# Optimization experiments

Measured on AMD Instinct MI355X. Metric: run time of the kernel, lower is better.

The kernel has to match this reference:

```python
import jax, jax.numpy as jnp
import numpy as np

NEG_SLOPE = 0.2  # PyG GATConv default negative_slope
EPS = 1e-16


def gat_conv(x, src, dst, num_nodes, W, att_src, att_dst, bias, concat):
    """PyG-style GATConv (eval mode, no dropout). att_*: [H, C]."""
    H, C = att_src.shape
    h = (x @ W).reshape(num_nodes, H, C)                      # [N,H,C]
    a_s = jnp.einsum('nhc,hc->nh', h, att_src)                # [N,H]
    a_d = jnp.einsum('nhc,hc->nh', h, att_dst)                # [N,H]
    e = jax.nn.leaky_relu(a_s[src] + a_d[dst], NEG_SLOPE)     # [E,H]
    # segment softmax over edges grouped by destination node
    m = jax.lax.stop_gradient(jax.ops.segment_max(e, dst, num_segments=num_nodes))
    ex = jnp.exp(e - m[dst])
    denom = jax.ops.segment_sum(ex, dst, num_segments=num_nodes)
    alpha = ex / (denom[dst] + EPS)                           # [E,H]
    msg = h[src] * alpha[:, :, None]                          # [E,H,C]
    out = jax.ops.segment_sum(msg, dst, num_segments=num_nodes)  # [N,H,C]
    out = out.reshape(num_nodes, H * C) if concat else out.mean(axis=1)
    return out + bias


def setup_inputs() -> dict:
    key = jax.random.key(0)
    ks = jax.random.split(key, 12)
    N, E = 65536, 1310720
    IN, HID, OUT, HEADS = 768, 128, 2, 8
    C1 = HID // HEADS  # 16
    s = 0.05
    return {
        'x': jax.random.normal(ks[0], (N, IN), jnp.float32),
        'edge_index': jax.random.randint(ks[1], (2, E), 0, N, jnp.int64),
        'W1': jax.random.normal(ks[2], (IN, HEADS * C1), jnp.float32) * s,
        'att_src1': jax.random.normal(ks[3], (HEADS, C1), jnp.float32) * s,
        'att_dst1': jax.random.normal(ks[4], (HEADS, C1), jnp.float32) * s,
        'b1': jnp.zeros((HID,), jnp.float32),
        'Wp': jax.random.normal(ks[5], (IN, HID), jnp.float32) * s,
        'bp': jnp.zeros((HID,), jnp.float32),
        'W2': jax.random.normal(ks[6], (HID, OUT), jnp.float32) * s,
        'att_src2': jax.random.normal(ks[7], (1, OUT), jnp.float32) * s,
        'att_dst2': jax.random.normal(ks[8], (1, OUT), jnp.float32) * s,
        'b2': jnp.zeros((OUT,), jnp.float32),
    }


def reference(x, edge_index, W1, att_src1, att_dst1, b1, Wp, bp, W2, att_src2, att_dst2, b2):
    N = x.shape[0]
    loops = jnp.arange(N, dtype=edge_index.dtype)  # add_self_loops=True
    src = jnp.concatenate([edge_index[0], loops])
    dst = jnp.concatenate([edge_index[1], loops])
    # eval mode: dropout is identity
    h1 = gat_conv(x, src, dst, N, W1, att_src1, att_dst1, b1, concat=True)
    h = jax.nn.elu(h1 + x @ Wp + bp)  # residual projection + ELU
    return gat_conv(h, src, dst, N, W2, att_src2, att_dst2, b2, concat=False)
```

## Files before the change

### kernel.cpp

```cpp
#include <hip/hip_runtime.h>
#include <hip/hip_bf16.h>
#include <math.h>

#define NEG_SLOPE 0.2f

typedef __attribute__((ext_vector_type(8))) short short8;
typedef __attribute__((ext_vector_type(4))) float float4v;

__device__ __forceinline__ unsigned f2bf(float f) {
  unsigned u = __builtin_bit_cast(unsigned, f);
  return (u + 0x7fffu + ((u >> 16) & 1u)) >> 16;
}
__device__ __forceinline__ float bflo(unsigned u) {
  return __builtin_bit_cast(float, u << 16);
}
__device__ __forceinline__ float bfhi(unsigned u) {
  return __builtin_bit_cast(float, u & 0xffff0000u);
}

__global__ __launch_bounds__(256) void convert_w(const float* __restrict__ W1,
                                                 const float* __restrict__ Wp,
                                                 short* __restrict__ Wt) {
  int k = blockIdx.x;
  int c = threadIdx.x;
  float v = (c < 128) ? W1[k * 128 + c] : Wp[k * 128 + (c - 128)];
  Wt[(size_t)c * 768 + k] = (short)f2bf(v);
}

__global__ __launch_bounds__(256) void gemm_mfma(const float* __restrict__ x,
                                                 const short* __restrict__ Wt,
                                                 float* __restrict__ proj,
                                                 unsigned* __restrict__ h1bf) {
  __shared__ short As[64][40];
  __shared__ short Bs[256][40];
  const int tid = threadIdx.x;
  const int wave = tid >> 6, lane = tid & 63;
  const int l15 = lane & 15, l4 = lane >> 4;
  const int row0 = blockIdx.x * 64;

  const int ar = tid >> 3;
  const int ak = (tid & 7) * 4;
  const int bc = tid >> 2;
  const int bk = (tid & 3) * 8;

  float4v acc[4][4] = {};

  for (int k0 = 0; k0 < 768; k0 += 32) {
#pragma unroll
    for (int i = 0; i < 2; i++) {
      int r = i * 32 + ar;
      float4 f = *(const float4*)&x[(size_t)(row0 + r) * 768 + k0 + ak];
      uint2 p;
      p.x = f2bf(f.x) | (f2bf(f.y) << 16);
      p.y = f2bf(f.z) | (f2bf(f.w) << 16);
      *(uint2*)&As[r][ak] = p;
    }
#pragma unroll
    for (int i = 0; i < 4; i++) {
      int c = i * 64 + bc;
      uint4 v = *(const uint4*)&Wt[(size_t)c * 768 + k0 + bk];
      *(uint4*)&Bs[c][bk] = v;
    }
    __syncthreads();

    short8 afr[4];
#pragma unroll
    for (int rt = 0; rt < 4; rt++)
      afr[rt] = *(const short8*)&As[rt * 16 + l15][l4 * 8];
#pragma unroll
    for (int ct = 0; ct < 4; ct++) {
      short8 bfr = *(const short8*)&Bs[wave * 64 + ct * 16 + l15][l4 * 8];
#pragma unroll
      for (int rt = 0; rt < 4; rt++)
        acc[rt][ct] =
            __builtin_amdgcn_mfma_f32_16x16x32_bf16(afr[rt], bfr, acc[rt][ct], 0, 0, 0);
    }
    __syncthreads();
  }

  const int colbase = wave * 64;
  if (wave < 2) {
#pragma unroll
    for (int ct = 0; ct < 4; ct++) {
      const int c = colbase + ct * 16 + l15;
#pragma unroll
      for (int rt = 0; rt < 4; rt++) {
#pragma unroll
        for (int r = 0; r < 4; r++) {
          const int R = row0 + rt * 16 + l4 * 4 + r;
          unsigned u = f2bf(acc[rt][ct][r]);
          unsigned up = __shfl_xor(u, 1);
          if ((l15 & 1) == 0) h1bf[(size_t)R * 64 + (c >> 1)] = u | (up << 16);
        }
      }
    }
  } else {
#pragma unroll
    for (int ct = 0; ct < 4; ct++) {
      const int c = colbase - 128 + ct * 16 + l15;
#pragma unroll
      for (int rt = 0; rt < 4; rt++) {
#pragma unroll
        for (int r = 0; r < 4; r++) {
          const int R = row0 + rt * 16 + l4 * 4 + r;
          proj[(size_t)R * 128 + c] = acc[rt][ct][r];
        }
      }
    }
  }
}

__global__ __launch_bounds__(256) void attn1b(const uint4* __restrict__ h1bf4,
                                              const float* __restrict__ att_src1,
                                              const float* __restrict__ att_dst1,
                                              float* __restrict__ a_s1,
                                              float* __restrict__ a_d1) {
  const int t = blockIdx.x * 256 + threadIdx.x;
  const int n = t >> 3, h = t & 7;
  uint4 q0 = h1bf4[(size_t)n * 16 + h * 2];
  uint4 q1 = h1bf4[(size_t)n * 16 + h * 2 + 1];
  float v[16];
  v[0] = bflo(q0.x); v[1] = bfhi(q0.x); v[2] = bflo(q0.y); v[3] = bfhi(q0.y);
  v[4] = bflo(q0.z); v[5] = bfhi(q0.z); v[6] = bflo(q0.w); v[7] = bfhi(q0.w);
  v[8] = bflo(q1.x); v[9] = bfhi(q1.x); v[10] = bflo(q1.y); v[11] = bfhi(q1.y);
  v[12] = bflo(q1.z); v[13] = bfhi(q1.z); v[14] = bflo(q1.w); v[15] = bfhi(q1.w);
  float as = 0.f, ad = 0.f;
#pragma unroll
  for (int i = 0; i < 16; i++) {
    as += v[i] * att_src1[h * 16 + i];
    ad += v[i] * att_dst1[h * 16 + i];
  }
  a_s1[t] = as;
  a_d1[t] = ad;
}

__global__ void init_counts(int* counts, int N) {
  int i = blockIdx.x * blockDim.x + threadIdx.x;
  if (i < N) counts[i] = 1;
}

__global__ void hist_kernel(const int* __restrict__ dst, int* counts, int E) {
  int i = blockIdx.x * blockDim.x + threadIdx.x;
  int base = i * 4;
  if (base + 3 < E) {
    int4 d = *(const int4*)&dst[base];
    atomicAdd(&counts[d.x], 1);
    atomicAdd(&counts[d.y], 1);
    atomicAdd(&counts[d.z], 1);
    atomicAdd(&counts[d.w], 1);
  } else {
    for (int j = base; j < E; j++) atomicAdd(&counts[dst[j]], 1);
  }
}

__global__ __launch_bounds__(256) void scan_a(const int* __restrict__ counts,
                                              int* offsets, int* bsum) {
  __shared__ int s[256];
  int t = threadIdx.x, idx = blockIdx.x * 256 + t;
  int v = counts[idx];
  s[t] = v;
  __syncthreads();
  for (int d = 1; d < 256; d <<= 1) {
    int x = (t >= d) ? s[t - d] : 0;
    __syncthreads();
    s[t] += x;
    __syncthreads();
  }
  offsets[idx] = s[t] - v;
  if (t == 255) bsum[blockIdx.x] = s[t];
}

__global__ __launch_bounds__(256) void scan_b(int* bsum) {
  __shared__ int s[256];
  int t = threadIdx.x;
  int v = bsum[t];
  s[t] = v;
  __syncthreads();
  for (int d = 1; d < 256; d <<= 1) {
    int x = (t >= d) ? s[t - d] : 0;
    __syncthreads();
    s[t] += x;
    __syncthreads();
  }
  bsum[t] = s[t] - v;
}

__global__ __launch_bounds__(256) void scan_c(int* offsets, const int* bsum,
                                              int* cursor, int* sortedsrc,
                                              int N, int Etot) {
  int t = threadIdx.x, idx = blockIdx.x * 256 + t;
  int off = offsets[idx] + bsum[blockIdx.x];
  offsets[idx] = off;
  sortedsrc[off] = idx;
  cursor[idx] = off + 1;
  if (idx == 0) offsets[N] = Etot;
}

__global__ void scatter_edges(const int* __restrict__ src,
                              const int* __restrict__ dst, int* cursor,
                              int* sortedsrc, int E) {
  int i = blockIdx.x * blockDim.x + threadIdx.x;
  int base = i * 4;
  if (base + 3 < E) {
    int4 s = *(const int4*)&src[base];
    int4 d = *(const int4*)&dst[base];
    sortedsrc[atomicAdd(&cursor[d.x], 1)] = s.x;
    sortedsrc[atomicAdd(&cursor[d.y], 1)] = s.y;
    sortedsrc[atomicAdd(&cursor[d.z], 1)] = s.z;
    sortedsrc[atomicAdd(&cursor[d.w], 1)] = s.w;
  } else {
    for (int j = base; j < E; j++)
      sortedsrc[atomicAdd(&cursor[dst[j]], 1)] = src[j];
  }
}

__global__ __launch_bounds__(256) void agg1_fused(
    const uint4* __restrict__ h1bf4, const float* __restrict__ proj,
    const float* __restrict__ a_s1, const float* __restrict__ a_d1,
    const int* __restrict__ offsets, const int* __restrict__ sortedsrc,
    const float* __restrict__ b1, const float* __restrict__ bp,
    const float* __restrict__ W2, const float* __restrict__ att_s2,
    const float* __restrict__ att_d2, float* __restrict__ h2,
    float* __restrict__ as2, float* __restrict__ ad2) {
  const int t = threadIdx.x;
  const int n = blockIdx.x * 16 + (t >> 4);
  const int k = t & 15;
  const int hd = k >> 1;
  const float ad = a_d1[n * 8 + hd];
  const int begin = offsets[n], end = offsets[n + 1];
  float acc[8] = {};
  float aw = 0.f;
  int j = begin;
  for (; j + 4 <= end; j += 4) {
    int s0 = sortedsrc[j], s1 = sortedsrc[j + 1];
    int s2 = sortedsrc[j + 2], s3 = sortedsrc[j + 3];
    float e0 = a_s1[s0 * 8 + hd], e1 = a_s1[s1 * 8 + hd];
    float e2 = a_s1[s2 * 8 + hd], e3 = a_s1[s3 * 8 + hd];
    uint4 q0 = h1bf4[(size_t)s0 * 16 + k];
    uint4 q1 = h1bf4[(size_t)s1 * 16 + k];
    uint4 q2 = h1bf4[(size_t)s2 * 16 + k];
    uint4 q3 = h1bf4[(size_t)s3 * 16 + k];
    e0 += ad; e1 += ad; e2 += ad; e3 += ad;
    float w0 = __expf(e0 > 0.f ? e0 : NEG_SLOPE * e0);
    float w1 = __expf(e1 > 0.f ? e1 : NEG_SLOPE * e1);
    float w2 = __expf(e2 > 0.f ? e2 : NEG_SLOPE * e2);
    float w3 = __expf(e3 > 0.f ? e3 : NEG_SLOPE * e3);
    acc[0] += w0 * bflo(q0.x) + w1 * bflo(q1.x) + w2 * bflo(q2.x) + w3 * bflo(q3.x);
    acc[1] += w0 * bfhi(q0.x) + w1 * bfhi(q1.x) + w2 * bfhi(q2.x) + w3 * bfhi(q3.x);
    acc[2] += w0 * bflo(q0.y) + w1 * bflo(q1.y) + w2 * bflo(q2.y) + w3 * bflo(q3.y);
    acc[3] += w0 * bfhi(q0.y) + w1 * bfhi(q1.y) + w2 * bfhi(q2.y) + w3 * bfhi(q3.y);
    acc[4] += w0 * bflo(q0.z) + w1 * bflo(q1.z) + w2 * bflo(q2.z) + w3 * bflo(q3.z);
    acc[5] += w0 * bfhi(q0.z) + w1 * bfhi(q1.z) + w2 * bfhi(q2.z) + w3 * bfhi(q3.z);
    acc[6] += w0 * bflo(q0.w) + w1 * bflo(q1.w) + w2 * bflo(q2.w) + w3 * bflo(q3.w);
    acc[7] += w0 * bfhi(q0.w) + w1 * bfhi(q1.w) + w2 * bfhi(q2.w) + w3 * bfhi(q3.w);
    aw += (w0 + w1) + (w2 + w3);
  }
  for (; j < end; j++) {
    int s0 = sortedsrc[j];
    float e0 = a_s1[s0 * 8 + hd] + ad;
    uint4 q0 = h1bf4[(size_t)s0 * 16 + k];
    float w0 = __expf(e0 > 0.f ? e0 : NEG_SLOPE * e0);
    acc[0] += w0 * bflo(q0.x);
    acc[1] += w0 * bfhi(q0.x);
    acc[2] += w0 * bflo(q0.y);
    acc[3] += w0 * bfhi(q0.y);
    acc[4] += w0 * bflo(q0.z);
    acc[5] += w0 * bfhi(q0.z);
    acc[6] += w0 * bflo(q0.w);
    acc[7] += w0 * bfhi(q0.w);
    aw += w0;
  }
  const float inv = 1.f / (aw + 1e-16f);
  const float4 pj0 = *(const float4*)&proj[(size_t)n * 128 + k * 8];
  const float4 pj1 = *(const float4*)&proj[(size_t)n * 128 + k * 8 + 4];
  const float4 b1a = *(const float4*)&b1[k * 8];
  const float4 b1b = *(const float4*)&b1[k * 8 + 4];
  const float4 bpa = *(const float4*)&bp[k * 8];
  const float4 bpb = *(const float4*)&bp[k * 8 + 4];
  float v[8];
  v[0] = acc[0] * inv + pj0.x + b1a.x + bpa.x;
  v[1] = acc[1] * inv + pj0.y + b1a.y + bpa.y;
  v[2] = acc[2] * inv + pj0.z + b1a.z + bpa.z;
  v[3] = acc[3] * inv + pj0.w + b1a.w + bpa.w;
  v[4] = acc[4] * inv + pj1.x + b1b.x + bpb.x;
  v[5] = acc[5] * inv + pj1.y + b1b.y + bpb.y;
  v[6] = acc[6] * inv + pj1.z + b1b.z + bpb.z;
  v[7] = acc[7] * inv + pj1.w + b1b.w + bpb.w;
  float p0 = 0.f, p1 = 0.f;
#pragma unroll
  for (int i = 0; i < 8; i++) {
    float vi = v[i] > 0.f ? v[i] : (__expf(v[i]) - 1.f);
    float2 w2 = *(const float2*)&W2[(k * 8 + i) * 2];
    p0 += vi * w2.x;
    p1 += vi * w2.y;
  }
#pragma unroll
  for (int off = 8; off; off >>= 1) {
    p0 += __shfl_xor(p0, off);
    p1 += __shfl_xor(p1, off);
  }
  if (k == 0) {
    h2[2 * n] = p0;
    h2[2 * n + 1] = p1;
    as2[n] = p0 * att_s2[0] + p1 * att_s2[1];
    ad2[n] = p0 * att_d2[0] + p1 * att_d2[1];
  }
}

__global__ __launch_bounds__(256) void agg2(
    const float* __restrict__ h2, const float* __restrict__ as2,
    const float* __restrict__ ad2, const int* __restrict__ offsets,
    const int* __restrict__ sortedsrc, const float* __restrict__ b2,
    float* __restrict__ out, int N) {
  const int node = blockIdx.x * 16 + (threadIdx.x >> 4);
  const int lane = threadIdx.x & 15;
  const int begin = offsets[node], end = offsets[node + 1];
  const float ad = ad2[node];
  float acc0 = 0.f, acc1 = 0.f, aw = 0.f;
  for (int j = begin + lane; j < end; j += 16) {
    int s = sortedsrc[j];
    float e = as2[s] + ad;
    float w = __expf(e > 0.f ? e : NEG_SLOPE * e);
    float2 hh = *(const float2*)&h2[2 * s];
    acc0 += w * hh.x;
    acc1 += w * hh.y;
    aw += w;
  }
#pragma unroll
  for (int off = 8; off; off >>= 1) {
    acc0 += __shfl_xor(acc0, off);
    acc1 += __shfl_xor(acc1, off);
    aw += __shfl_xor(aw, off);
  }
  if (lane == 0) {
    float inv = 1.f / (aw + 1e-16f);
    out[2 * node] = acc0 * inv + b2[0];
    out[2 * node + 1] = acc1 * inv + b2[1];
  }
}

extern "C" void kernel_launch(void* const* d_in, const int* in_sizes, int n_in,
                              void* d_out, int out_size, void* d_ws,
                              size_t ws_size, hipStream_t stream) {
  const float* x = (const float*)d_in[0];
  const int* edge_index = (const int*)d_in[1];
  const float* W1 = (const float*)d_in[2];
  const float* att_src1 = (const float*)d_in[3];
  const float* att_dst1 = (const float*)d_in[4];
  const float* b1 = (const float*)d_in[5];
  const float* Wp = (const float*)d_in[6];
  const float* bp = (const float*)d_in[7];
  const float* W2 = (const float*)d_in[8];
  const float* att_src2 = (const float*)d_in[9];
  const float* att_dst2 = (const float*)d_in[10];
  const float* b2 = (const float*)d_in[11];
  float* out = (float*)d_out;

  const int N = in_sizes[0] / 768;
  const int E = in_sizes[1] / 2;
  const int Etot = E + N;
  const int* src = edge_index;
  const int* dst = edge_index + E;

  char* ws = (char*)d_ws;
  size_t off = 0;
  auto alloc = [&](size_t bytes) {
    size_t cur = off;
    off += (bytes + 255) & ~(size_t)255;
    return (void*)(ws + cur);
  };
  float* proj = (float*)alloc((size_t)N * 128 * 4);
  unsigned* h1bf = (unsigned*)alloc((size_t)N * 64 * 4);
  float* a_s1 = (float*)alloc((size_t)N * 8 * 4);
  float* a_d1 = (float*)alloc((size_t)N * 8 * 4);
  float* h2 = (float*)alloc((size_t)N * 2 * 4);
  float* as2 = (float*)alloc((size_t)N * 4);
  float* ad2 = (float*)alloc((size_t)N * 4);
  int* counts = (int*)alloc((size_t)N * 4);
  int* offsets = (int*)alloc(((size_t)N + 1) * 4);
  int* cursor = (int*)alloc((size_t)N * 4);
  int* bsum = (int*)alloc(256 * 4);
  int* sortedsrc = (int*)alloc((size_t)Etot * 4);
  short* Wt = (short*)alloc((size_t)256 * 768 * 2);

  convert_w<<<768, 256, 0, stream>>>(W1, Wp, Wt);
  gemm_mfma<<<N / 64, 256, 0, stream>>>(x, Wt, proj, h1bf);
  attn1b<<<N * 8 / 256, 256, 0, stream>>>((const uint4*)h1bf, att_src1,
                                          att_dst1, a_s1, a_d1);
  init_counts<<<(N + 255) / 256, 256, 0, stream>>>(counts, N);
  hist_kernel<<<(E / 4 + 255) / 256, 256, 0, stream>>>(dst, counts, E);
  scan_a<<<N / 256, 256, 0, stream>>>(counts, offsets, bsum);
  scan_b<<<1, 256, 0, stream>>>(bsum);
  scan_c<<<N / 256, 256, 0, stream>>>(offsets, bsum, cursor, sortedsrc, N,
                                      Etot);
  scatter_edges<<<(E / 4 + 255) / 256, 256, 0, stream>>>(src, dst, cursor,
                                                         sortedsrc, E);
  agg1_fused<<<N / 16, 256, 0, stream>>>((const uint4*)h1bf, proj, a_s1, a_d1,
                                         offsets, sortedsrc, b1, bp, W2,
                                         att_src2, att_dst2, h2, as2, ad2);
  agg2<<<N / 16, 256, 0, stream>>>(h2, as2, ad2, offsets, sortedsrc, b2, out,
                                   N);
}
```

Before: 568.1 us.

## Load GEMM tiles directly into LDS and fold small setup kernels

The MFMA GEMM now uses global_load_lds to copy fp32 x tiles and bf16 weight tiles straight into shared memory in a lane-linear layout. The fp32-to-bf16 conversion moves to the point where A fragments are read from LDS. This is meant to cut register staging and VGPR traffic on the load path, at the cost of twice the LDS footprint for A. The counts initialisation is merged into convert_w, and the block-sum scan is merged into scan_c, which recomputes the prefix in every block. Together these remove two kernel launches.

```diff
diff --git a/kernel.cpp b/kernel.cpp
--- a/kernel.cpp
+++ b/kernel.cpp
@@ -18,58 +18,70 @@
   return __builtin_bit_cast(float, u & 0xffff0000u);
 }
 
+#define GLD16(gp, lp)                                                         \
+  __builtin_amdgcn_global_load_lds(                                           \
+      (const __attribute__((address_space(1))) void*)(gp),                    \
+      (__attribute__((address_space(3))) void*)(lp), 16, 0, 0)
+
 __global__ __launch_bounds__(256) void convert_w(const float* __restrict__ W1,
                                                  const float* __restrict__ Wp,
-                                                 short* __restrict__ Wt) {
+                                                 short* __restrict__ Wt,
+                                                 int* __restrict__ counts,
+                                                 int N) {
   int k = blockIdx.x;
   int c = threadIdx.x;
   float v = (c < 128) ? W1[k * 128 + c] : Wp[k * 128 + (c - 128)];
   Wt[(size_t)c * 768 + k] = (short)f2bf(v);
+  int i = blockIdx.x * 256 + threadIdx.x;
+  if (i < N) counts[i] = 1;
 }
 
 __global__ __launch_bounds__(256) void gemm_mfma(const float* __restrict__ x,
                                                  const short* __restrict__ Wt,
                                                  float* __restrict__ proj,
                                                  unsigned* __restrict__ h1bf) {
-  __shared__ short As[64][40];
-  __shared__ short Bs[256][40];
+  __shared__ float As[2048];
+  __shared__ short Bs[8192];
   const int tid = threadIdx.x;
   const int wave = tid >> 6, lane = tid & 63;
   const int l15 = lane & 15, l4 = lane >> 4;
   const int row0 = blockIdx.x * 64;
 
-  const int ar = tid >> 3;
-  const int ak = (tid & 7) * 4;
-  const int bc = tid >> 2;
-  const int bk = (tid & 3) * 8;
-
   float4v acc[4][4] = {};
 
   for (int k0 = 0; k0 < 768; k0 += 32) {
 #pragma unroll
-    for (int i = 0; i < 2; i++) {
-      int r = i * 32 + ar;
-      float4 f = *(const float4*)&x[(size_t)(row0 + r) * 768 + k0 + ak];
-      uint2 p;
-      p.x = f2bf(f.x) | (f2bf(f.y) << 16);
-      p.y = f2bf(f.z) | (f2bf(f.w) << 16);
-      *(uint2*)&As[r][ak] = p;
-    }
-#pragma unroll
-    for (int i = 0; i < 4; i++) {
-      int c = i * 64 + bc;
-      uint4 v = *(const uint4*)&Wt[(size_t)c * 768 + k0 + bk];
-      *(uint4*)&Bs[c][bk] = v;
+    for (int s = 0; s < 2; s++) {
+      const int ia = wave * 2 + s;
+      const int rt = ia >> 1, kcg = (ia & 1) * 4;
+      const int kc = kcg + l4, r = l15;
+      const float* gp = x + (size_t)(row0 + rt * 16 + r) * 768 + k0 + kc * 4;
+      GLD16(gp, As + ia * 256);
+    }
+#pragma unroll
+    for (int s = 0; s < 4; s++) {
+      const int cb = wave * 4 + s;
+      const short* gp = Wt + (size_t)(cb * 16 + l15) * 768 + k0 + l4 * 8;
+      GLD16(gp, Bs + cb * 512);
     }
     __syncthreads();
 
     short8 afr[4];
 #pragma unroll
-    for (int rt = 0; rt < 4; rt++)
-      afr[rt] = *(const short8*)&As[rt * 16 + l15][l4 * 8];
+    for (int rt = 0; rt < 4; rt++) {
+      float4 fa = *(const float4*)&As[((rt * 8 + 2 * l4) * 16 + l15) * 4];
+      float4 fb = *(const float4*)&As[((rt * 8 + 2 * l4 + 1) * 16 + l15) * 4];
+      uint4 pk;
+      pk.x = f2bf(fa.x) | (f2bf(fa.y) << 16);
+      pk.y = f2bf(fa.z) | (f2bf(fa.w) << 16);
+      pk.z = f2bf(fb.x) | (f2bf(fb.y) << 16);
+      pk.w = f2bf(fb.z) | (f2bf(fb.w) << 16);
+      afr[rt] = __builtin_bit_cast(short8, pk);
+    }
 #pragma unroll
     for (int ct = 0; ct < 4; ct++) {
-      short8 bfr = *(const short8*)&Bs[wave * 64 + ct * 16 + l15][l4 * 8];
+      const int cb = wave * 4 + ct;
+      short8 bfr = *(const short8*)&Bs[((cb * 4 + l4) * 16 + l15) * 8];
 #pragma unroll
       for (int rt = 0; rt < 4; rt++)
         acc[rt][ct] =
@@ -134,11 +146,6 @@
   a_d1[t] = ad;
 }
 
-__global__ void init_counts(int* counts, int N) {
-  int i = blockIdx.x * blockDim.x + threadIdx.x;
-  if (i < N) counts[i] = 1;
-}
-
 __global__ void hist_kernel(const int* __restrict__ dst, int* counts, int E) {
   int i = blockIdx.x * blockDim.x + threadIdx.x;
   int base = i * 4;
@@ -170,11 +177,13 @@
   if (t == 255) bsum[blockIdx.x] = s[t];
 }
 
-__global__ __launch_bounds__(256) void scan_b(int* bsum) {
+__global__ __launch_bounds__(256) void scan_c(int* offsets,
+                                              const int* __restrict__ bsum,
+                                              int* cursor, int* sortedsrc,
+                                              int N, int Etot) {
   __shared__ int s[256];
-  int t = threadIdx.x;
-  int v = bsum[t];
-  s[t] = v;
+  int t = threadIdx.x, idx = blockIdx.x * 256 + t;
+  s[t] = bsum[t];
   __syncthreads();
   for (int d = 1; d < 256; d <<= 1) {
     int x = (t >= d) ? s[t - d] : 0;
@@ -182,14 +191,8 @@
     s[t] += x;
     __syncthreads();
   }
-  bsum[t] = s[t] - v;
-}
-
-__global__ __launch_bounds__(256) void scan_c(int* offsets, const int* bsum,
-                                              int* cursor, int* sortedsrc,
-                                              int N, int Etot) {
-  int t = threadIdx.x, idx = blockIdx.x * 256 + t;
-  int off = offsets[idx] + bsum[blockIdx.x];
+  int blockpref = (blockIdx.x == 0) ? 0 : s[blockIdx.x - 1];
+  int off = offsets[idx] + blockpref;
   offsets[idx] = off;
   sortedsrc[off] = idx;
   cursor[idx] = off + 1;
@@ -383,14 +386,12 @@
   int* sortedsrc = (int*)alloc((size_t)Etot * 4);
   short* Wt = (short*)alloc((size_t)256 * 768 * 2);
 
-  convert_w<<<768, 256, 0, stream>>>(W1, Wp, Wt);
+  convert_w<<<768, 256, 0, stream>>>(W1, Wp, Wt, counts, N);
   gemm_mfma<<<N / 64, 256, 0, stream>>>(x, Wt, proj, h1bf);
   attn1b<<<N * 8 / 256, 256, 0, stream>>>((const uint4*)h1bf, att_src1,
                                           att_dst1, a_s1, a_d1);
-  init_counts<<<(N + 255) / 256, 256, 0, stream>>>(counts, N);
   hist_kernel<<<(E / 4 + 255) / 256, 256, 0, stream>>>(dst, counts, E);
   scan_a<<<N / 256, 256, 0, stream>>>(counts, offsets, bsum);
-  scan_b<<<1, 256, 0, stream>>>(bsum);
   scan_c<<<N / 256, 256, 0, stream>>>(offsets, bsum, cursor, sortedsrc, N,
                                       Etot);
   scatter_edges<<<(E / 4 + 255) / 256, 256, 0, stream>>>(src, dst, cursor,
```

New measurement: 578.7 us. No clear change (+1.9%).
